# Kernel optimization log

Measured on AMD Instinct MI355X. Metric: run time of the kernel, lower is better.

Reference implementation:

```python
import jax, jax.numpy as jnp
import numpy as np

N_NODES = 50000


def gcn_conv(x, W, b, src, dst):
    # PyG GCNConv: lin (no bias) -> add self-loops -> symmetric deg norm ->
    # scatter-add messages to target nodes -> add bias.
    n = x.shape[0]
    xw = x @ W  # [N, H]
    loops = jnp.arange(n, dtype=src.dtype)
    s = jnp.concatenate([src, loops])
    d = jnp.concatenate([dst, loops])
    deg = jax.ops.segment_sum(jnp.ones(d.shape[0], dtype=x.dtype), d, num_segments=n)
    dinv = deg ** -0.5  # deg >= 1 due to self-loops
    norm = dinv[s] * dinv[d]  # [E+N]
    msg = xw[s] * norm[:, None]  # gather + scale, [E+N, H]
    out = jax.ops.segment_sum(msg, d, num_segments=n)  # scatter-add
    return out + b


def setup_inputs() -> dict:
    key = jax.random.key(0)
    ks = jax.random.split(key, 8)
    in_feats, hidden, out_feats, p = 64, 64, 32, 4
    x = jax.random.normal(ks[0], (N_NODES, in_feats), dtype=jnp.float32)
    edge_index = jax.random.randint(ks[1], (2, 800000), 0, N_NODES, dtype=jnp.int64)
    s1 = (1.0 / in_feats) ** 0.5
    s2 = (1.0 / hidden) ** 0.5
    W1 = jax.random.uniform(ks[2], (in_feats, hidden), jnp.float32, -s1, s1)
    b1 = jnp.zeros((hidden,), jnp.float32)
    W2 = jax.random.uniform(ks[3], (hidden, hidden), jnp.float32, -s2, s2)
    b2 = jnp.zeros((hidden,), jnp.float32)
    Wr = jax.random.uniform(ks[4], (hidden, out_feats * p), jnp.float32, -s2, s2)
    br = jax.random.uniform(ks[5], (out_feats * p,), jnp.float32, -s2, s2)
    return {"x": x, "edge_index": edge_index, "W1": W1, "b1": b1,
            "W2": W2, "b2": b2, "Wr": Wr, "br": br}


def reference(x, edge_index, W1, b1, W2, b2, Wr, br):
    src, dst = edge_index[0], edge_index[1]
    h = jax.nn.relu(gcn_conv(x, W1, b1, src, dst))
    h = jax.nn.relu(gcn_conv(h, W2, b2, src, dst))
    g = jnp.mean(h, axis=0, keepdims=True)  # [1, hidden]
    out = (g @ Wr + br).reshape(32, 4)  # (out_feats, p)
    return out
```

## Files before the change

### kernel.cpp

```cpp
#include <hip/hip_runtime.h>
#include <math.h>


#define CH 4096
#define MAXNB 1024

__device__ __forceinline__ float bf2f(unsigned short u) {
    return __uint_as_float(((unsigned)u) << 16);
}
__device__ __forceinline__ unsigned short f2bf(float x) {
    unsigned b = __float_as_uint(x);
    return (unsigned short)((b + 0x7FFF + ((b >> 16) & 1)) >> 16);
}

__global__ __launch_bounds__(256) void k_bucket_hist(const int* __restrict__ dst,
                                                     int* __restrict__ histmat,
                                                     int E, int NB) {
    __shared__ int ih[MAXNB];
    int t = threadIdx.x;
    for (int k = t; k < NB; k += 256) ih[k] = 0;
    __syncthreads();
    int base = blockIdx.x * CH;
    for (int i = 0; i < CH; i += 256) {
        int e = base + i + t;
        if (e < E) atomicAdd(&ih[dst[e] >> 6], 1);
    }
    __syncthreads();
    for (int k = t; k < NB; k += 256) histmat[(size_t)blockIdx.x * NB + k] = ih[k];
}

__global__ __launch_bounds__(1024) void k_scan(int* __restrict__ histmat,
                                               int* __restrict__ bstart,
                                               int* __restrict__ offsets,
                                               float* __restrict__ g,
                                               int NB, int nch, int E, int n) {
    __shared__ int sc[1024];
    int t = threadIdx.x;
    int run = 0;
    if (t < NB) {
        int b = 0;
        for (; b + 8 <= nch; b += 8) {
            int v[8];
#pragma unroll
            for (int u = 0; u < 8; u++) v[u] = histmat[(size_t)(b + u) * NB + t];
#pragma unroll
            for (int u = 0; u < 8; u++) {
                int x = v[u];
                histmat[(size_t)(b + u) * NB + t] = run;
                run += x;
            }
        }
        for (; b < nch; b++) {
            int x = histmat[(size_t)b * NB + t];
            histmat[(size_t)b * NB + t] = run;
            run += x;
        }
    }
    sc[t] = (t < NB) ? run : 0;
    __syncthreads();
    for (int off = 1; off < 1024; off <<= 1) {
        int x = (t >= off) ? sc[t - off] : 0;
        __syncthreads();
        sc[t] += x;
        __syncthreads();
    }
    if (t < NB) bstart[t] = sc[t] - run;
    if (t == 0) { bstart[NB] = E; offsets[n] = E; }
    if (t < 64) g[t] = 0.f;
}

__global__ __launch_bounds__(256) void k_bucket_scatter(const int* __restrict__ src,
                                                        const int* __restrict__ dst,
                                                        const int* __restrict__ histmat,
                                                        const int* __restrict__ bstart,
                                                        int* __restrict__ staged,
                                                        int E, int NB) {
    __shared__ int cur[MAXNB];
    int t = threadIdx.x;
    for (int k = t; k < NB; k += 256)
        cur[k] = bstart[k] + histmat[(size_t)blockIdx.x * NB + k];
    __syncthreads();
    int base = blockIdx.x * CH;
    for (int i = 0; i < CH; i += 256) {
        int e = base + i + t;
        if (e < E) {
            int d = dst[e];
            int pos = atomicAdd(&cur[d >> 6], 1);
            staged[pos] = (src[e] << 6) | (d & 63);
        }
    }
}

__global__ __launch_bounds__(256) void k_local_sort(const int* __restrict__ staged,
                                                    const int* __restrict__ bstart,
                                                    unsigned short* __restrict__ csr,
                                                    int* __restrict__ offsets,
                                                    float* __restrict__ dinv, int n) {
    __shared__ int cnt[64];
    __shared__ int pos[64];
    __shared__ int cur[64];
    int t = threadIdx.x;
    if (t < 64) cnt[t] = 0;
    __syncthreads();
    int k = blockIdx.x;
    int beg = bstart[k], end = bstart[k + 1];
    for (int e = beg + t; e < end; e += 256) atomicAdd(&cnt[staged[e] & 63], 1);
    __syncthreads();
    if (t == 0) {
        int run = 0;
        for (int i = 0; i < 64; i++) { pos[i] = run; run += cnt[i]; }
    }
    __syncthreads();
    if (t < 64) {
        cur[t] = pos[t];
        int node = k * 64 + t;
        if (node < n) {
            offsets[node] = beg + pos[t];
            dinv[node] = 1.0f / sqrtf((float)(cnt[t] + 1));
        }
    }
    __syncthreads();
    for (int e = beg + t; e < end; e += 256) {
        int pk = staged[e];
        int p = atomicAdd(&cur[pk & 63], 1);
        csr[beg + p] = (unsigned short)(pk >> 6);
    }
}

__global__ __launch_bounds__(256) void k_gemm_scale(const float* __restrict__ X,
                                                    const float* __restrict__ W,
                                                    const float* __restrict__ dinv,
                                                    unsigned short* __restrict__ Y, int n) {
    __shared__ float Ws[64 * 64];
    __shared__ float xs[16][64];
    int t = threadIdx.x, w = t >> 6, f = t & 63;
    const float4* W4 = (const float4*)W;
    float4* Ws4 = (float4*)Ws;
#pragma unroll
    for (int j = 0; j < 4; j++) Ws4[t + 256 * j] = W4[t + 256 * j];
    int r0 = blockIdx.x * 16;
#pragma unroll
    for (int i = 0; i < 4; i++) {
        int r = r0 + w * 4 + i;
        xs[w * 4 + i][f] = (r < n) ? X[(size_t)r * 64 + f] : 0.f;
    }
    __syncthreads();
    float acc[4] = {0.f, 0.f, 0.f, 0.f};
#pragma unroll 8
    for (int k = 0; k < 64; k++) {
        float wv = Ws[k * 64 + f];
#pragma unroll
        for (int i = 0; i < 4; i++) acc[i] += xs[w * 4 + i][k] * wv;
    }
#pragma unroll
    for (int i = 0; i < 4; i++) {
        int r = r0 + w * 4 + i;
        if (r < n) Y[(size_t)r * 64 + f] = f2bf(dinv[r] * acc[i]);
    }
}

__global__ __launch_bounds__(256) void k_agg_fuse(const unsigned short* __restrict__ Y,
                                                  const float* __restrict__ dinv,
                                                  const float* __restrict__ bias,
                                                  const int* __restrict__ offsets,
                                                  const unsigned short* __restrict__ csr,
                                                  const float* __restrict__ W2,
                                                  unsigned short* __restrict__ Yout, int n) {
    __shared__ float Ws[64 * 64];
    __shared__ float hs[4][64];
    const ushort4* Y4 = (const ushort4*)Y;
    int t = threadIdx.x, w = t >> 6, l = t & 63;
    int q = l >> 4, c = l & 15;
    {
        const float4* W4 = (const float4*)W2;
        float4* Ws4 = (float4*)Ws;
#pragma unroll
        for (int j = 0; j < 4; j++) Ws4[t + 256 * j] = W4[t + 256 * j];
    }
    int node = blockIdx.x * 4 + w;
    bool valid = node < n;
    float4 hval = make_float4(0.f, 0.f, 0.f, 0.f);
    float dv = 0.f;
    if (valid) {
        float4 acc = make_float4(0.f, 0.f, 0.f, 0.f);
        if (q == 0) {
            ushort4 u = Y4[(size_t)node * 16 + c];
            acc = make_float4(bf2f(u.x), bf2f(u.y), bf2f(u.z), bf2f(u.w));
        }
        int beg = offsets[node], end = offsets[node + 1];
        for (int j = beg + q; j < end; j += 16) {
#pragma unroll
            for (int u = 0; u < 4; u++) {
                int jj = j + 4 * u;
                if (jj < end) {
                    int s = csr[jj];
                    ushort4 v = Y4[(size_t)s * 16 + c];
                    acc.x += bf2f(v.x); acc.y += bf2f(v.y);
                    acc.z += bf2f(v.z); acc.w += bf2f(v.w);
                }
            }
        }
#pragma unroll
        for (int m = 16; m <= 32; m <<= 1) {
            acc.x += __shfl_xor(acc.x, m);
            acc.y += __shfl_xor(acc.y, m);
            acc.z += __shfl_xor(acc.z, m);
            acc.w += __shfl_xor(acc.w, m);
        }
        dv = dinv[node];
        float4 b4 = ((const float4*)bias)[c];
        hval.x = fmaxf(dv * acc.x + b4.x, 0.f);
        hval.y = fmaxf(dv * acc.y + b4.y, 0.f);
        hval.z = fmaxf(dv * acc.z + b4.z, 0.f);
        hval.w = fmaxf(dv * acc.w + b4.w, 0.f);
    }
    if (q == 0) ((float4*)hs[w])[c] = hval;
    __syncthreads();
    if (valid) {
        float acc2 = 0.f;
#pragma unroll
        for (int m = 0; m < 16; m++) {
            float4 h4 = ((const float4*)hs[w])[m];
            acc2 += h4.x * Ws[(4 * m + 0) * 64 + l] + h4.y * Ws[(4 * m + 1) * 64 + l]
                  + h4.z * Ws[(4 * m + 2) * 64 + l] + h4.w * Ws[(4 * m + 3) * 64 + l];
        }
        Yout[(size_t)node * 64 + l] = f2bf(dv * acc2);
    }
}

__global__ __launch_bounds__(256) void k_agg_pool(const unsigned short* __restrict__ Y,
                                                  const float* __restrict__ dinv,
                                                  const float* __restrict__ bias,
                                                  const int* __restrict__ offsets,
                                                  const unsigned short* __restrict__ csr,
                                                  float* __restrict__ pbuf, int n) {
    __shared__ float4 sm4[4][16];
    const ushort4* Y4 = (const ushort4*)Y;
    int t = threadIdx.x, w = t >> 6, l = t & 63;
    int q = l >> 4, c = l & 15;
    int node = blockIdx.x * 4 + w;
    bool valid = node < n;
    float4 hval = make_float4(0.f, 0.f, 0.f, 0.f);
    if (valid) {
        float4 acc = make_float4(0.f, 0.f, 0.f, 0.f);
        if (q == 0) {
            ushort4 u = Y4[(size_t)node * 16 + c];
            acc = make_float4(bf2f(u.x), bf2f(u.y), bf2f(u.z), bf2f(u.w));
        }
        int beg = offsets[node], end = offsets[node + 1];
        for (int j = beg + q; j < end; j += 16) {
#pragma unroll
            for (int u = 0; u < 4; u++) {
                int jj = j + 4 * u;
                if (jj < end) {
                    int s = csr[jj];
                    ushort4 v = Y4[(size_t)s * 16 + c];
                    acc.x += bf2f(v.x); acc.y += bf2f(v.y);
                    acc.z += bf2f(v.z); acc.w += bf2f(v.w);
                }
            }
        }
#pragma unroll
        for (int m = 16; m <= 32; m <<= 1) {
            acc.x += __shfl_xor(acc.x, m);
            acc.y += __shfl_xor(acc.y, m);
            acc.z += __shfl_xor(acc.z, m);
            acc.w += __shfl_xor(acc.w, m);
        }
        float dv = dinv[node];
        float4 b4 = ((const float4*)bias)[c];
        hval.x = fmaxf(dv * acc.x + b4.x, 0.f);
        hval.y = fmaxf(dv * acc.y + b4.y, 0.f);
        hval.z = fmaxf(dv * acc.z + b4.z, 0.f);
        hval.w = fmaxf(dv * acc.w + b4.w, 0.f);
    }
    if (q == 0) sm4[w][c] = valid ? hval : make_float4(0.f, 0.f, 0.f, 0.f);
    __syncthreads();
    if (t < 16) {
        float4 a = sm4[0][t], b = sm4[1][t], d = sm4[2][t], e = sm4[3][t];
        float4 s;
        s.x = (a.x + b.x) + (d.x + e.x);
        s.y = (a.y + b.y) + (d.y + e.y);
        s.z = (a.z + b.z) + (d.z + e.z);
        s.w = (a.w + b.w) + (d.w + e.w);
        ((float4*)pbuf)[(size_t)blockIdx.x * 16 + t] = s;
    }
}

__global__ void k_mean_final(const float* __restrict__ pbuf, float* __restrict__ g,
                             int nrows) {
    __shared__ float part[256];
    int t = threadIdx.x, w = t >> 6, f = t & 63;
    float local = 0.f;
    for (int r = blockIdx.x * 4 + w; r < nrows; r += gridDim.x * 4)
        local += pbuf[(size_t)r * 64 + f];
    part[t] = local;
    __syncthreads();
    if (w == 0) {
        float tot = part[f] + part[64 + f] + part[128 + f] + part[192 + f];
        atomicAdd(&g[f], tot);
    }
}

__global__ void k_readout(const float* __restrict__ g, const float* __restrict__ Wr,
                          const float* __restrict__ br, float* __restrict__ out,
                          float invn) {
    __shared__ float gl[64];
    int t = threadIdx.x;
    if (t < 64) gl[t] = g[t] * invn;
    __syncthreads();
    float acc = br[t];
#pragma unroll
    for (int k = 0; k < 64; k++) acc += gl[k] * Wr[k * 128 + t];
    out[t] = acc;
}

extern "C" void kernel_launch(void* const* d_in, const int* in_sizes, int n_in,
                              void* d_out, int out_size, void* d_ws, size_t ws_size,
                              hipStream_t stream) {
    const float* x  = (const float*)d_in[0];
    const int*   ei = (const int*)d_in[1];
    const float* W1 = (const float*)d_in[2];
    const float* b1 = (const float*)d_in[3];
    const float* W2 = (const float*)d_in[4];
    const float* b2 = (const float*)d_in[5];
    const float* Wr = (const float*)d_in[6];
    const float* br = (const float*)d_in[7];
    float* out = (float*)d_out;

    int n = in_sizes[0] / 64;
    int E = in_sizes[1] / 2;
    const int* src = ei;
    const int* dst = ei + E;

    int NB  = (n + 63) / 64;
    int nch = (E + CH - 1) / CH;

    char* p = (char*)d_ws;
    unsigned short* y1 = (unsigned short*)p; p += (size_t)n * 64 * sizeof(unsigned short);
    unsigned short* y2 = (unsigned short*)p; p += (size_t)n * 64 * sizeof(unsigned short);
    float* pbuf = (float*)p;   p += (size_t)((n + 3) / 4) * 64 * sizeof(float);
    float* dinv = (float*)p;   p += (size_t)n * sizeof(float);
    float* g = (float*)p;      p += 64 * sizeof(float);
    int* staged = (int*)p;     p += (size_t)E * sizeof(int);
    int* offsets = (int*)p;    p += (size_t)(n + 1) * sizeof(int);
    int* histmat = (int*)p;    p += (size_t)nch * NB * sizeof(int);
    int* bstart = (int*)p;     p += (size_t)(NB + 1) * sizeof(int);
    unsigned short* csr = (unsigned short*)p; p += (size_t)E * sizeof(unsigned short);

    k_bucket_hist<<<nch, 256, 0, stream>>>(dst, histmat, E, NB);
    k_scan<<<1, 1024, 0, stream>>>(histmat, bstart, offsets, g, NB, nch, E, n);
    k_bucket_scatter<<<nch, 256, 0, stream>>>(src, dst, histmat, bstart, staged, E, NB);
    k_local_sort<<<NB, 256, 0, stream>>>(staged, bstart, csr, offsets, dinv, n);

    int gb = (n + 3) / 4;
    k_gemm_scale<<<(n + 15) / 16, 256, 0, stream>>>(x, W1, dinv, y1, n);
    k_agg_fuse<<<gb, 256, 0, stream>>>(y1, dinv, b1, offsets, csr, W2, y2, n);
    k_agg_pool<<<gb, 256, 0, stream>>>(y2, dinv, b2, offsets, csr, pbuf, n);

    k_mean_final<<<64, 256, 0, stream>>>(pbuf, g, gb);
    k_readout<<<1, 128, 0, stream>>>(g, Wr, br, out, 1.0f / (float)n);
}
```

Baseline: 229.9 us.

## Process two nodes per wavefront in aggregation kernels and halve bucket chunk size

Each wavefront in the two aggregation kernels now gathers neighbours for two consecutive nodes at once, interleaving their edge loads to raise memory-level parallelism. In the fused kernel this also amortises each W2 shared-memory read over two output rows, and the block count and the per-block W2 staging into shared memory are halved. The bucket-sort chunk size CH is also halved, which doubles the number of histogram/scatter blocks. The costs are higher register pressure, and load imbalance when the two nodes have different degrees.

```diff
diff --git a/kernel.cpp b/kernel.cpp
--- a/kernel.cpp
+++ b/kernel.cpp
@@ -2,7 +2,7 @@
 #include <math.h>
 
 
-#define CH 4096
+#define CH 2048
 #define MAXNB 1024
 
 __device__ __forceinline__ float bf2f(unsigned short u) {
@@ -159,6 +159,51 @@
     }
 }
 
+__device__ __forceinline__ void xorred(float4& a, int m) {
+    a.x += __shfl_xor(a.x, m);
+    a.y += __shfl_xor(a.y, m);
+    a.z += __shfl_xor(a.z, m);
+    a.w += __shfl_xor(a.w, m);
+}
+
+#define GATHER2(Y4, offsets, csr, nA, nB, vA, vB, accA, accB)                 \
+    {                                                                         \
+        int begA = 0, endA = 0, begB = 0, endB = 0;                           \
+        if (vA) { begA = offsets[nA]; endA = offsets[nA + 1]; }               \
+        if (vB) { begB = offsets[nB]; endB = offsets[nB + 1]; }               \
+        if (vA && q == 0) {                                                   \
+            ushort4 u = Y4[(size_t)nA * 16 + c];                              \
+            accA = make_float4(bf2f(u.x), bf2f(u.y), bf2f(u.z), bf2f(u.w));   \
+        }                                                                     \
+        if (vB && q == 0) {                                                   \
+            ushort4 u = Y4[(size_t)nB * 16 + c];                              \
+            accB = make_float4(bf2f(u.x), bf2f(u.y), bf2f(u.z), bf2f(u.w));   \
+        }                                                                     \
+        int jA = begA + q, jB = begB + q;                                     \
+        while (jA < endA || jB < endB) {                                      \
+            _Pragma("unroll")                                                 \
+            for (int u = 0; u < 4; u++) {                                     \
+                int ja = jA + 4 * u;                                          \
+                if (ja < endA) {                                              \
+                    int s = csr[ja];                                          \
+                    ushort4 v = Y4[(size_t)s * 16 + c];                       \
+                    accA.x += bf2f(v.x); accA.y += bf2f(v.y);                 \
+                    accA.z += bf2f(v.z); accA.w += bf2f(v.w);                 \
+                }                                                             \
+                int jb = jB + 4 * u;                                          \
+                if (jb < endB) {                                              \
+                    int s = csr[jb];                                          \
+                    ushort4 v = Y4[(size_t)s * 16 + c];                       \
+                    accB.x += bf2f(v.x); accB.y += bf2f(v.y);                 \
+                    accB.z += bf2f(v.z); accB.w += bf2f(v.w);                 \
+                }                                                             \
+            }                                                                 \
+            jA += 16; jB += 16;                                               \
+        }                                                                     \
+        xorred(accA, 16); xorred(accA, 32);                                   \
+        xorred(accB, 16); xorred(accB, 32);                                   \
+    }
+
 __global__ __launch_bounds__(256) void k_agg_fuse(const unsigned short* __restrict__ Y,
                                                   const float* __restrict__ dinv,
                                                   const float* __restrict__ bias,
@@ -167,7 +212,7 @@
                                                   const float* __restrict__ W2,
                                                   unsigned short* __restrict__ Yout, int n) {
     __shared__ float Ws[64 * 64];
-    __shared__ float hs[4][64];
+    __shared__ float hs[4][2][64];
     const ushort4* Y4 = (const ushort4*)Y;
     int t = threadIdx.x, w = t >> 6, l = t & 63;
     int q = l >> 4, c = l & 15;
@@ -177,55 +222,41 @@
 #pragma unroll
         for (int j = 0; j < 4; j++) Ws4[t + 256 * j] = W4[t + 256 * j];
     }
-    int node = blockIdx.x * 4 + w;
-    bool valid = node < n;
-    float4 hval = make_float4(0.f, 0.f, 0.f, 0.f);
-    float dv = 0.f;
-    if (valid) {
-        float4 acc = make_float4(0.f, 0.f, 0.f, 0.f);
-        if (q == 0) {
-            ushort4 u = Y4[(size_t)node * 16 + c];
-            acc = make_float4(bf2f(u.x), bf2f(u.y), bf2f(u.z), bf2f(u.w));
-        }
-        int beg = offsets[node], end = offsets[node + 1];
-        for (int j = beg + q; j < end; j += 16) {
-#pragma unroll
-            for (int u = 0; u < 4; u++) {
-                int jj = j + 4 * u;
-                if (jj < end) {
-                    int s = csr[jj];
-                    ushort4 v = Y4[(size_t)s * 16 + c];
-                    acc.x += bf2f(v.x); acc.y += bf2f(v.y);
-                    acc.z += bf2f(v.z); acc.w += bf2f(v.w);
-                }
-            }
-        }
-#pragma unroll
-        for (int m = 16; m <= 32; m <<= 1) {
-            acc.x += __shfl_xor(acc.x, m);
-            acc.y += __shfl_xor(acc.y, m);
-            acc.z += __shfl_xor(acc.z, m);
-            acc.w += __shfl_xor(acc.w, m);
-        }
-        dv = dinv[node];
-        float4 b4 = ((const float4*)bias)[c];
-        hval.x = fmaxf(dv * acc.x + b4.x, 0.f);
-        hval.y = fmaxf(dv * acc.y + b4.y, 0.f);
-        hval.z = fmaxf(dv * acc.z + b4.z, 0.f);
-        hval.w = fmaxf(dv * acc.w + b4.w, 0.f);
-    }
-    if (q == 0) ((float4*)hs[w])[c] = hval;
-    __syncthreads();
-    if (valid) {
-        float acc2 = 0.f;
-#pragma unroll
-        for (int m = 0; m < 16; m++) {
-            float4 h4 = ((const float4*)hs[w])[m];
-            acc2 += h4.x * Ws[(4 * m + 0) * 64 + l] + h4.y * Ws[(4 * m + 1) * 64 + l]
-                  + h4.z * Ws[(4 * m + 2) * 64 + l] + h4.w * Ws[(4 * m + 3) * 64 + l];
-        }
-        Yout[(size_t)node * 64 + l] = f2bf(dv * acc2);
-    }
+    int nA = (blockIdx.x * 4 + w) * 2;
+    int nB = nA + 1;
+    bool vA = nA < n, vB = nB < n;
+    float4 accA = make_float4(0.f, 0.f, 0.f, 0.f);
+    float4 accB = make_float4(0.f, 0.f, 0.f, 0.f);
+    GATHER2(Y4, offsets, csr, nA, nB, vA, vB, accA, accB);
+    float dvA = vA ? dinv[nA] : 0.f;
+    float dvB = vB ? dinv[nB] : 0.f;
+    float4 b4 = ((const float4*)bias)[c];
+    float4 hA, hB;
+    hA.x = fmaxf(dvA * accA.x + b4.x, 0.f);
+    hA.y = fmaxf(dvA * accA.y + b4.y, 0.f);
+    hA.z = fmaxf(dvA * accA.z + b4.z, 0.f);
+    hA.w = fmaxf(dvA * accA.w + b4.w, 0.f);
+    hB.x = fmaxf(dvB * accB.x + b4.x, 0.f);
+    hB.y = fmaxf(dvB * accB.y + b4.y, 0.f);
+    hB.z = fmaxf(dvB * accB.z + b4.z, 0.f);
+    hB.w = fmaxf(dvB * accB.w + b4.w, 0.f);
+    if (q == 0) {
+        ((float4*)hs[w][0])[c] = hA;
+        ((float4*)hs[w][1])[c] = hB;
+    }
+    __syncthreads();
+    float a2A = 0.f, a2B = 0.f;
+#pragma unroll
+    for (int m = 0; m < 16; m++) {
+        float4 xA = ((const float4*)hs[w][0])[m];
+        float4 xB = ((const float4*)hs[w][1])[m];
+        float w0 = Ws[(4 * m + 0) * 64 + l], w1 = Ws[(4 * m + 1) * 64 + l];
+        float w2 = Ws[(4 * m + 2) * 64 + l], w3 = Ws[(4 * m + 3) * 64 + l];
+        a2A += xA.x * w0 + xA.y * w1 + xA.z * w2 + xA.w * w3;
+        a2B += xB.x * w0 + xB.y * w1 + xB.z * w2 + xB.w * w3;
+    }
+    if (vA) Yout[(size_t)nA * 64 + l] = f2bf(dvA * a2A);
+    if (vB) Yout[(size_t)nB * 64 + l] = f2bf(dvB * a2B);
 }
 
 __global__ __launch_bounds__(256) void k_agg_pool(const unsigned short* __restrict__ Y,
@@ -238,52 +269,34 @@
     const ushort4* Y4 = (const ushort4*)Y;
     int t = threadIdx.x, w = t >> 6, l = t & 63;
     int q = l >> 4, c = l & 15;
-    int node = blockIdx.x * 4 + w;
-    bool valid = node < n;
-    float4 hval = make_float4(0.f, 0.f, 0.f, 0.f);
-    if (valid) {
-        float4 acc = make_float4(0.f, 0.f, 0.f, 0.f);
-        if (q == 0) {
-            ushort4 u = Y4[(size_t)node * 16 + c];
-            acc = make_float4(bf2f(u.x), bf2f(u.y), bf2f(u.z), bf2f(u.w));
-        }
-        int beg = offsets[node], end = offsets[node + 1];
-        for (int j = beg + q; j < end; j += 16) {
-#pragma unroll
-            for (int u = 0; u < 4; u++) {
-                int jj = j + 4 * u;
-                if (jj < end) {
-                    int s = csr[jj];
-                    ushort4 v = Y4[(size_t)s * 16 + c];
-                    acc.x += bf2f(v.x); acc.y += bf2f(v.y);
-                    acc.z += bf2f(v.z); acc.w += bf2f(v.w);
-                }
-            }
-        }
-#pragma unroll
-        for (int m = 16; m <= 32; m <<= 1) {
-            acc.x += __shfl_xor(acc.x, m);
-            acc.y += __shfl_xor(acc.y, m);
-            acc.z += __shfl_xor(acc.z, m);
-            acc.w += __shfl_xor(acc.w, m);
-        }
-        float dv = dinv[node];
-        float4 b4 = ((const float4*)bias)[c];
-        hval.x = fmaxf(dv * acc.x + b4.x, 0.f);
-        hval.y = fmaxf(dv * acc.y + b4.y, 0.f);
-        hval.z = fmaxf(dv * acc.z + b4.z, 0.f);
-        hval.w = fmaxf(dv * acc.w + b4.w, 0.f);
-    }
-    if (q == 0) sm4[w][c] = valid ? hval : make_float4(0.f, 0.f, 0.f, 0.f);
+    int nA = (blockIdx.x * 4 + w) * 2;
+    int nB = nA + 1;
+    bool vA = nA < n, vB = nB < n;
+    float4 accA = make_float4(0.f, 0.f, 0.f, 0.f);
+    float4 accB = make_float4(0.f, 0.f, 0.f, 0.f);
+    GATHER2(Y4, offsets, csr, nA, nB, vA, vB, accA, accB);
+    float dvA = vA ? dinv[nA] : 0.f;
+    float dvB = vB ? dinv[nB] : 0.f;
+    float4 b4 = ((const float4*)bias)[c];
+    float4 s;
+    s.x = (vA ? fmaxf(dvA * accA.x + b4.x, 0.f) : 0.f)
+        + (vB ? fmaxf(dvB * accB.x + b4.x, 0.f) : 0.f);
+    s.y = (vA ? fmaxf(dvA * accA.y + b4.y, 0.f) : 0.f)
+        + (vB ? fmaxf(dvB * accB.y + b4.y, 0.f) : 0.f);
+    s.z = (vA ? fmaxf(dvA * accA.z + b4.z, 0.f) : 0.f)
+        + (vB ? fmaxf(dvB * accB.z + b4.z, 0.f) : 0.f);
+    s.w = (vA ? fmaxf(dvA * accA.w + b4.w, 0.f) : 0.f)
+        + (vB ? fmaxf(dvB * accB.w + b4.w, 0.f) : 0.f);
+    if (q == 0) sm4[w][c] = s;
     __syncthreads();
     if (t < 16) {
         float4 a = sm4[0][t], b = sm4[1][t], d = sm4[2][t], e = sm4[3][t];
-        float4 s;
-        s.x = (a.x + b.x) + (d.x + e.x);
-        s.y = (a.y + b.y) + (d.y + e.y);
-        s.z = (a.z + b.z) + (d.z + e.z);
-        s.w = (a.w + b.w) + (d.w + e.w);
-        ((float4*)pbuf)[(size_t)blockIdx.x * 16 + t] = s;
+        float4 o;
+        o.x = (a.x + b.x) + (d.x + e.x);
+        o.y = (a.y + b.y) + (d.y + e.y);
+        o.z = (a.z + b.z) + (d.z + e.z);
+        o.w = (a.w + b.w) + (d.w + e.w);
+        ((float4*)pbuf)[(size_t)blockIdx.x * 16 + t] = o;
     }
 }
 
@@ -339,7 +352,7 @@
     char* p = (char*)d_ws;
     unsigned short* y1 = (unsigned short*)p; p += (size_t)n * 64 * sizeof(unsigned short);
     unsigned short* y2 = (unsigned short*)p; p += (size_t)n * 64 * sizeof(unsigned short);
-    float* pbuf = (float*)p;   p += (size_t)((n + 3) / 4) * 64 * sizeof(float);
+    float* pbuf = (float*)p;   p += (size_t)((n + 7) / 8) * 64 * sizeof(float);
     float* dinv = (float*)p;   p += (size_t)n * sizeof(float);
     float* g = (float*)p;      p += 64 * sizeof(float);
     int* staged = (int*)p;     p += (size_t)E * sizeof(int);
@@ -353,11 +366,11 @@
     k_bucket_scatter<<<nch, 256, 0, stream>>>(src, dst, histmat, bstart, staged, E, NB);
     k_local_sort<<<NB, 256, 0, stream>>>(staged, bstart, csr, offsets, dinv, n);
 
-    int gb = (n + 3) / 4;
+    int gb2 = (n + 7) / 8;
     k_gemm_scale<<<(n + 15) / 16, 256, 0, stream>>>(x, W1, dinv, y1, n);
-    k_agg_fuse<<<gb, 256, 0, stream>>>(y1, dinv, b1, offsets, csr, W2, y2, n);
-    k_agg_pool<<<gb, 256, 0, stream>>>(y2, dinv, b2, offsets, csr, pbuf, n);
-
-    k_mean_final<<<64, 256, 0, stream>>>(pbuf, g, gb);
+    k_agg_fuse<<<gb2, 256, 0, stream>>>(y1, dinv, b1, offsets, csr, W2, y2, n);
+    k_agg_pool<<<gb2, 256, 0, stream>>>(y2, dinv, b2, offsets, csr, pbuf, n);
+
+    k_mean_final<<<64, 256, 0, stream>>>(pbuf, g, gb2);
     k_readout<<<1, 128, 0, stream>>>(g, Wr, br, out, 1.0f / (float)n);
 }
```

Measured after the change: 272.8 us. +18.6%, slower.
